# Optimization experiments

Measured on AMD Instinct MI355X. Metric: run time of the kernel, lower is better.

The kernel has to match this reference:

```python
import jax, jax.numpy as jnp
import numpy as np

R_SELF = 0.1  # config.r_self from the 'GENERAL' preset


def setup_inputs() -> dict:
    key = jax.random.key(0)
    k1, k2 = jax.random.split(key)
    N, M, D = 16384, 8192, 128
    x = jax.random.uniform(k1, (N, D), dtype=jnp.float32)
    self_samples = jax.random.uniform(k2, (M, D), dtype=jnp.float32)
    return {"x": x, "self_samples": self_samples}


def _cdist(a, b):
    # Euclidean pairwise distances, same math as torch.cdist(p=2).
    a2 = jnp.sum(a * a, axis=1, keepdims=True)          # [N,1]
    b2 = jnp.sum(b * b, axis=1)[None, :]                # [1,M]
    d2 = a2 + b2 - 2.0 * (a @ b.T)                      # [N,M]
    return jnp.sqrt(jnp.maximum(d2, 0.0))


def reference(x, self_samples):
    # get_anomaly_score: min over self set, shifted by r_self, clamped at 0.
    min_dist_to_self = jnp.min(_cdist(x, self_samples), axis=1)  # [N]
    score = jnp.maximum(min_dist_to_self - R_SELF, 0.0)
    return score
```

## Files before the change

kernel.cpp:

```cpp
#include <hip/hip_runtime.h>


using half_t = _Float16;
typedef _Float16 half8 __attribute__((ext_vector_type(8)));
typedef float floatx16 __attribute__((ext_vector_type(16)));

#define TILE_ELEMS (128 * 128)

__device__ __forceinline__ void async_load16(const void* g, void* l) {
    __builtin_amdgcn_global_load_lds(
        (const __attribute__((address_space(1))) void*)g,
        (__attribute__((address_space(3))) void*)l, 16, 0, 0);
}

__global__ __launch_bounds__(256) void prep_kernel(
    const float* __restrict__ x, const float* __restrict__ self,
    half_t* __restrict__ Aws, half_t* __restrict__ Bws,
    float* __restrict__ b2h, float* __restrict__ a2, int Atiles)
{
    __shared__ float part[256];
    int tile = blockIdx.x;
    int tid  = threadIdx.x;
    bool isB = tile >= Atiles;
    int bt   = tile - Atiles;
    const float* src = isB ? (self + (size_t)bt * TILE_ELEMS)
                           : (x    + (size_t)tile * TILE_ELEMS);
    half_t* dst = isB ? (Bws + (size_t)bt * TILE_ELEMS)
                      : (Aws + (size_t)tile * TILE_ELEMS);
    float sgn = isB ? 1.f : -1.f;

    int rowt = tid & 127;
    int k8b  = tid >> 7;
    float ss = 0.f;
    #pragma unroll
    for (int i = 0; i < 8; ++i) {
        int k8 = i * 2 + k8b;
        const float4* p = (const float4*)(src + rowt * 128 + k8 * 8);
        float4 f0 = p[0];
        float4 f1 = p[1];
        half8 h;
        h[0] = (half_t)(sgn * f0.x); h[1] = (half_t)(sgn * f0.y);
        h[2] = (half_t)(sgn * f0.z); h[3] = (half_t)(sgn * f0.w);
        h[4] = (half_t)(sgn * f1.x); h[5] = (half_t)(sgn * f1.y);
        h[6] = (half_t)(sgn * f1.z); h[7] = (half_t)(sgn * f1.w);
        *(half8*)(dst + (size_t)(i * 256 + tid) * 8) = h;
        ss += f0.x*f0.x + f0.y*f0.y + f0.z*f0.z + f0.w*f0.w;
        ss += f1.x*f1.x + f1.y*f1.y + f1.z*f1.z + f1.w*f1.w;
    }
    part[tid] = ss;
    __syncthreads();
    if (tid < 128) {
        float tot = part[tid] + part[tid + 128];
        if (isB) b2h[bt * 128 + tid] = 0.5f * tot;
        else     a2[tile * 128 + tid] = tot;
    }
}

__global__ __launch_bounds__(256, 2) void min_gemm_kernel(
    const half_t* __restrict__ Aws, const half_t* __restrict__ Bws,
    const float* __restrict__ b2h, float* __restrict__ Pmin,
    int Mslice)
{
    __shared__ half_t Bsh[2][TILE_ELEMS];

    int tid  = threadIdx.x;
    int lane = tid & 63;
    int wid  = tid >> 6;
    int wr   = wid >> 1, wc = wid & 1;
    int ln31 = lane & 31, lh = lane >> 5;

    const half_t* Atile = Aws + (size_t)blockIdx.x * TILE_ELEMS;
    half8 areg[2][8];
    #pragma unroll
    for (int rt = 0; rt < 2; ++rt)
        #pragma unroll
        for (int ki = 0; ki < 8; ++ki) {
            int k8  = ki * 2 + lh;
            int row = wr * 64 + rt * 32 + ln31;
            areg[rt][ki] = *(const half8*)(Atile + (size_t)(k8 * 128 + row) * 8);
        }

    float minacc[2][16];
    #pragma unroll
    for (int rt = 0; rt < 2; ++rt)
        #pragma unroll
        for (int r = 0; r < 16; ++r) minacc[rt][r] = 1e30f;

    int iters = Mslice >> 7;
    int s = blockIdx.y;
    const half_t* Bbase = Bws + (size_t)s * iters * TILE_ELEMS;

    #pragma unroll
    for (int j = 0; j < 8; ++j) {
        int seg = wid * 8 + j;
        async_load16(Bbase + (size_t)(seg * 64 + lane) * 8,
                     &Bsh[0][(size_t)seg * 512]);
    }
    __syncthreads();

    float b2v0 = b2h[s * Mslice + wc * 64 + ln31];
    float b2v1 = b2h[s * Mslice + wc * 64 + 32 + ln31];

    int cur = 0;
    for (int it = 0; it < iters; ++it) {
        if (it + 1 < iters) {
            const half_t* Bt = Bbase + (size_t)(it + 1) * TILE_ELEMS;
            #pragma unroll
            for (int j = 0; j < 8; ++j) {
                int seg = wid * 8 + j;
                async_load16(Bt + (size_t)(seg * 64 + lane) * 8,
                             &Bsh[cur ^ 1][(size_t)seg * 512]);
            }
        }
        int nit = (it + 1 < iters) ? it + 1 : it;
        float nb0 = b2h[s * Mslice + nit * 128 + wc * 64 + ln31];
        float nb1 = b2h[s * Mslice + nit * 128 + wc * 64 + 32 + ln31];

        floatx16 c0, c1;
        #pragma unroll
        for (int r = 0; r < 16; ++r) { c0[r] = b2v0; c1[r] = b2v1; }

        const half_t* Bs = &Bsh[cur][0];

        floatx16 acc00, acc01, acc10, acc11;
        {
            int k8 = lh;
            half8 bf0 = *(const half8*)(Bs + (size_t)(k8 * 128 + wc * 64 + ln31) * 8);
            half8 bf1 = *(const half8*)(Bs + (size_t)(k8 * 128 + wc * 64 + 32 + ln31) * 8);
            acc00 = __builtin_amdgcn_mfma_f32_32x32x16_f16(areg[0][0], bf0, c0, 0, 0, 0);
            acc01 = __builtin_amdgcn_mfma_f32_32x32x16_f16(areg[0][0], bf1, c1, 0, 0, 0);
            acc10 = __builtin_amdgcn_mfma_f32_32x32x16_f16(areg[1][0], bf0, c0, 0, 0, 0);
            acc11 = __builtin_amdgcn_mfma_f32_32x32x16_f16(areg[1][0], bf1, c1, 0, 0, 0);
        }
        #pragma unroll
        for (int ki = 1; ki < 8; ++ki) {
            int k8 = ki * 2 + lh;
            half8 bf0 = *(const half8*)(Bs + (size_t)(k8 * 128 + wc * 64 + ln31) * 8);
            half8 bf1 = *(const half8*)(Bs + (size_t)(k8 * 128 + wc * 64 + 32 + ln31) * 8);
            acc00 = __builtin_amdgcn_mfma_f32_32x32x16_f16(areg[0][ki], bf0, acc00, 0, 0, 0);
            acc01 = __builtin_amdgcn_mfma_f32_32x32x16_f16(areg[0][ki], bf1, acc01, 0, 0, 0);
            acc10 = __builtin_amdgcn_mfma_f32_32x32x16_f16(areg[1][ki], bf0, acc10, 0, 0, 0);
            acc11 = __builtin_amdgcn_mfma_f32_32x32x16_f16(areg[1][ki], bf1, acc11, 0, 0, 0);
        }

        #pragma unroll
        for (int r = 0; r < 16; ++r) {
            minacc[0][r] = fminf(fminf(acc00[r], acc01[r]), minacc[0][r]);
            minacc[1][r] = fminf(fminf(acc10[r], acc11[r]), minacc[1][r]);
        }

        b2v0 = nb0; b2v1 = nb1;

        __syncthreads();
        cur ^= 1;
    }

    #pragma unroll
    for (int rt = 0; rt < 2; ++rt)
        #pragma unroll
        for (int r = 0; r < 16; ++r) {
            float v = minacc[rt][r];
            #pragma unroll
            for (int m = 1; m < 32; m <<= 1)
                v = fminf(v, __shfl_xor(v, m, 64));
            if (ln31 == 0) {
                int row = blockIdx.x * 128 + wr * 64 + rt * 32
                        + (r & 3) + 8 * (r >> 2) + 4 * lh;
                Pmin[(size_t)row * 8 + s * 2 + wc] = v;
            }
        }
}

__global__ __launch_bounds__(256) void final_kernel(
    const float* __restrict__ a2, const float* __restrict__ Pmin,
    float* __restrict__ out)
{
    int row = blockIdx.x * 256 + threadIdx.x;
    const float4* pp = (const float4*)(Pmin + (size_t)row * 8);
    float4 p0 = pp[0];
    float4 p1 = pp[1];
    float p = fminf(fminf(fminf(p0.x, p0.y), fminf(p0.z, p0.w)),
                    fminf(fminf(p1.x, p1.y), fminf(p1.z, p1.w)));
    float d2 = a2[row] + 2.f * p;
    float d  = sqrtf(fmaxf(d2, 0.f));
    out[row] = fmaxf(d - 0.1f, 0.f);
}

extern "C" void kernel_launch(void* const* d_in, const int* in_sizes, int n_in,
                              void* d_out, int out_size, void* d_ws, size_t ws_size,
                              hipStream_t stream)
{
    const float* x    = (const float*)d_in[0];
    const float* self = (const float*)d_in[1];
    float* out        = (float*)d_out;

    int N = in_sizes[0] / 128;
    int M = in_sizes[1] / 128;
    int Atiles = N / 128;
    int Btiles = M / 128;

    char* w      = (char*)d_ws;
    half_t* Aws  = (half_t*)w;
    half_t* Bws  = Aws + (size_t)N * 128;
    float*  b2h  = (float*)(w + (size_t)(N + M) * 128 * 2);
    float*  Pmin = b2h + M;
    float*  a2   = Pmin + (size_t)N * 8;

    prep_kernel<<<Atiles + Btiles, 256, 0, stream>>>(x, self, Aws, Bws, b2h, a2, Atiles);

    int Mslice = M / 4;
    dim3 grid(Atiles, 4);
    min_gemm_kernel<<<grid, 256, 0, stream>>>(Aws, Bws, b2h, Pmin, Mslice);

    final_kernel<<<N / 256, 256, 0, stream>>>(a2, Pmin, out);
}
```

Baseline: 102.3 us.

## Load B fragments directly from global into registers, dropping LDS double buffer

Removes the shared-memory double-buffered B tile staging (async global-to-LDS loads plus barriers) and has each wave read its B fragments straight from global memory into registers each iteration. This eliminates LDS traffic and block-wide synchronisation, and frees 64KB of LDS per block, which could allow more resident blocks. In exchange, B is fetched redundantly by the waves that share columns and is no longer prefetched ahead of use, so global and cache latency is exposed unless occupancy hides it.

Measured after the change: 114.0 us. 11.4% more time.

```diff
diff --git a/kernel.cpp b/kernel.cpp
--- a/kernel.cpp
+++ b/kernel.cpp
@@ -6,12 +6,6 @@
 typedef float floatx16 __attribute__((ext_vector_type(16)));
 
 #define TILE_ELEMS (128 * 128)
-
-__device__ __forceinline__ void async_load16(const void* g, void* l) {
-    __builtin_amdgcn_global_load_lds(
-        (const __attribute__((address_space(1))) void*)g,
-        (__attribute__((address_space(3))) void*)l, 16, 0, 0);
-}
 
 __global__ __launch_bounds__(256) void prep_kernel(
     const float* __restrict__ x, const float* __restrict__ self,
@@ -61,8 +55,6 @@
     const float* __restrict__ b2h, float* __restrict__ Pmin,
     int Mslice)
 {
-    __shared__ half_t Bsh[2][TILE_ELEMS];
-
     int tid  = threadIdx.x;
     int lane = tid & 63;
     int wid  = tid >> 6;
@@ -90,57 +82,36 @@
     int s = blockIdx.y;
     const half_t* Bbase = Bws + (size_t)s * iters * TILE_ELEMS;
 
-    #pragma unroll
-    for (int j = 0; j < 8; ++j) {
-        int seg = wid * 8 + j;
-        async_load16(Bbase + (size_t)(seg * 64 + lane) * 8,
-                     &Bsh[0][(size_t)seg * 512]);
-    }
-    __syncthreads();
+    for (int it = 0; it < iters; ++it) {
+        const half_t* Bt = Bbase + (size_t)it * TILE_ELEMS;
 
-    float b2v0 = b2h[s * Mslice + wc * 64 + ln31];
-    float b2v1 = b2h[s * Mslice + wc * 64 + 32 + ln31];
+        half8 bf0[8], bf1[8];
+        #pragma unroll
+        for (int ki = 0; ki < 8; ++ki) {
+            int k8 = ki * 2 + lh;
+            bf0[ki] = *(const half8*)(Bt + (size_t)(k8 * 128 + wc * 64 + ln31) * 8);
+            bf1[ki] = *(const half8*)(Bt + (size_t)(k8 * 128 + wc * 64 + 32 + ln31) * 8);
+        }
 
-    int cur = 0;
-    for (int it = 0; it < iters; ++it) {
-        if (it + 1 < iters) {
-            const half_t* Bt = Bbase + (size_t)(it + 1) * TILE_ELEMS;
-            #pragma unroll
-            for (int j = 0; j < 8; ++j) {
-                int seg = wid * 8 + j;
-                async_load16(Bt + (size_t)(seg * 64 + lane) * 8,
-                             &Bsh[cur ^ 1][(size_t)seg * 512]);
-            }
-        }
-        int nit = (it + 1 < iters) ? it + 1 : it;
-        float nb0 = b2h[s * Mslice + nit * 128 + wc * 64 + ln31];
-        float nb1 = b2h[s * Mslice + nit * 128 + wc * 64 + 32 + ln31];
+        int colbase = s * Mslice + it * 128 + wc * 64 + ln31;
+        float b2v0 = b2h[colbase];
+        float b2v1 = b2h[colbase + 32];
 
         floatx16 c0, c1;
         #pragma unroll
         for (int r = 0; r < 16; ++r) { c0[r] = b2v0; c1[r] = b2v1; }
 
-        const half_t* Bs = &Bsh[cur][0];
-
         floatx16 acc00, acc01, acc10, acc11;
-        {
-            int k8 = lh;
-            half8 bf0 = *(const half8*)(Bs + (size_t)(k8 * 128 + wc * 64 + ln31) * 8);
-            half8 bf1 = *(const half8*)(Bs + (size_t)(k8 * 128 + wc * 64 + 32 + ln31) * 8);
-            acc00 = __builtin_amdgcn_mfma_f32_32x32x16_f16(areg[0][0], bf0, c0, 0, 0, 0);
-            acc01 = __builtin_amdgcn_mfma_f32_32x32x16_f16(areg[0][0], bf1, c1, 0, 0, 0);
-            acc10 = __builtin_amdgcn_mfma_f32_32x32x16_f16(areg[1][0], bf0, c0, 0, 0, 0);
-            acc11 = __builtin_amdgcn_mfma_f32_32x32x16_f16(areg[1][0], bf1, c1, 0, 0, 0);
-        }
+        acc00 = __builtin_amdgcn_mfma_f32_32x32x16_f16(areg[0][0], bf0[0], c0, 0, 0, 0);
+        acc01 = __builtin_amdgcn_mfma_f32_32x32x16_f16(areg[0][0], bf1[0], c1, 0, 0, 0);
+        acc10 = __builtin_amdgcn_mfma_f32_32x32x16_f16(areg[1][0], bf0[0], c0, 0, 0, 0);
+        acc11 = __builtin_amdgcn_mfma_f32_32x32x16_f16(areg[1][0], bf1[0], c1, 0, 0, 0);
         #pragma unroll
         for (int ki = 1; ki < 8; ++ki) {
-            int k8 = ki * 2 + lh;
-            half8 bf0 = *(const half8*)(Bs + (size_t)(k8 * 128 + wc * 64 + ln31) * 8);
-            half8 bf1 = *(const half8*)(Bs + (size_t)(k8 * 128 + wc * 64 + 32 + ln31) * 8);
-            acc00 = __builtin_amdgcn_mfma_f32_32x32x16_f16(areg[0][ki], bf0, acc00, 0, 0, 0);
-            acc01 = __builtin_amdgcn_mfma_f32_32x32x16_f16(areg[0][ki], bf1, acc01, 0, 0, 0);
-            acc10 = __builtin_amdgcn_mfma_f32_32x32x16_f16(areg[1][ki], bf0, acc10, 0, 0, 0);
-            acc11 = __builtin_amdgcn_mfma_f32_32x32x16_f16(areg[1][ki], bf1, acc11, 0, 0, 0);
+            acc00 = __builtin_amdgcn_mfma_f32_32x32x16_f16(areg[0][ki], bf0[ki], acc00, 0, 0, 0);
+            acc01 = __builtin_amdgcn_mfma_f32_32x32x16_f16(areg[0][ki], bf1[ki], acc01, 0, 0, 0);
+            acc10 = __builtin_amdgcn_mfma_f32_32x32x16_f16(areg[1][ki], bf0[ki], acc10, 0, 0, 0);
+            acc11 = __builtin_amdgcn_mfma_f32_32x32x16_f16(areg[1][ki], bf1[ki], acc11, 0, 0, 0);
         }
 
         #pragma unroll
@@ -148,11 +119,6 @@
             minacc[0][r] = fminf(fminf(acc00[r], acc01[r]), minacc[0][r]);
             minacc[1][r] = fminf(fminf(acc10[r], acc11[r]), minacc[1][r]);
         }
-
-        b2v0 = nb0; b2v1 = nb1;
-
-        __syncthreads();
-        cur ^= 1;
     }
 
     #pragma unroll
```

## Use 512-thread blocks sharing B tiles via a triple-buffered LDS ring

Applied to the files above, without the earlier changes.

Each block now covers 256 A rows with 8 waves, so every staged B tile serves twice as many rows, which halves B traffic per row. B tiles go through a 3-deep LDS ring with explicit vmcnt waits and a single barrier per iteration, keeping two tiles in flight. The b2 slice is also preloaded into LDS once per block. In exchange, LDS use rises to about 104KB per block, which can limit occupancy to one block per CU despite launch_bounds(512,2).

Measured after the change: 100.2 us. 2.1% less time.

```diff
diff --git a/kernel.cpp b/kernel.cpp
--- a/kernel.cpp
+++ b/kernel.cpp
@@ -11,6 +11,15 @@
     __builtin_amdgcn_global_load_lds(
         (const __attribute__((address_space(1))) void*)g,
         (__attribute__((address_space(3))) void*)l, 16, 0, 0);
+}
+
+__device__ __forceinline__ void stage_tile(const half_t* __restrict__ Bt,
+                                           half_t* __restrict__ dst, int tid) {
+    #pragma unroll
+    for (int j = 0; j < 4; ++j) {
+        int chunk = j * 512 + tid;
+        async_load16(Bt + (size_t)chunk * 8, dst + (size_t)chunk * 8);
+    }
 }
 
 __global__ __launch_bounds__(256) void prep_kernel(
@@ -56,12 +65,63 @@
     }
 }
 
-__global__ __launch_bounds__(256, 2) void min_gemm_kernel(
+template<int VN>
+__device__ __forceinline__ void gemm_iter(
+    int t, int iters, int tid, int wc, int ln31, int lh,
+    const half_t* __restrict__ Bbase, half_t (*ring)[TILE_ELEMS],
+    const float* __restrict__ b2sh,
+    const half8 (&areg)[2][8], float (&minacc)[2][16])
+{
+    __builtin_amdgcn_sched_barrier(0);
+    if constexpr (VN == 4) asm volatile("s_waitcnt vmcnt(4)" ::: "memory");
+    else                   asm volatile("s_waitcnt vmcnt(0)" ::: "memory");
+    asm volatile("s_waitcnt lgkmcnt(0)" ::: "memory");
+    __builtin_amdgcn_s_barrier();
+    __builtin_amdgcn_sched_barrier(0);
+
+    if (t + 2 < iters)
+        stage_tile(Bbase + (size_t)(t + 2) * TILE_ELEMS, &ring[(t + 2) % 3][0], tid);
+
+    const half_t* Bs = &ring[t % 3][0];
+    float b2v0 = b2sh[t * 128 + wc * 64 + ln31];
+    float b2v1 = b2sh[t * 128 + wc * 64 + 32 + ln31];
+
+    floatx16 c0, c1;
+    #pragma unroll
+    for (int r = 0; r < 16; ++r) { c0[r] = b2v0; c1[r] = b2v1; }
+
+    floatx16 acc00, acc01, acc10, acc11;
+    {
+        half8 bf0 = *(const half8*)(Bs + (size_t)(lh * 128 + wc * 64 + ln31) * 8);
+        half8 bf1 = *(const half8*)(Bs + (size_t)(lh * 128 + wc * 64 + 32 + ln31) * 8);
+        acc00 = __builtin_amdgcn_mfma_f32_32x32x16_f16(areg[0][0], bf0, c0, 0, 0, 0);
+        acc01 = __builtin_amdgcn_mfma_f32_32x32x16_f16(areg[0][0], bf1, c1, 0, 0, 0);
+        acc10 = __builtin_amdgcn_mfma_f32_32x32x16_f16(areg[1][0], bf0, c0, 0, 0, 0);
+        acc11 = __builtin_amdgcn_mfma_f32_32x32x16_f16(areg[1][0], bf1, c1, 0, 0, 0);
+    }
+    #pragma unroll
+    for (int ki = 1; ki < 8; ++ki) {
+        half8 bf0 = *(const half8*)(Bs + (size_t)((ki * 2 + lh) * 128 + wc * 64 + ln31) * 8);
+        half8 bf1 = *(const half8*)(Bs + (size_t)((ki * 2 + lh) * 128 + wc * 64 + 32 + ln31) * 8);
+        acc00 = __builtin_amdgcn_mfma_f32_32x32x16_f16(areg[0][ki], bf0, acc00, 0, 0, 0);
+        acc01 = __builtin_amdgcn_mfma_f32_32x32x16_f16(areg[0][ki], bf1, acc01, 0, 0, 0);
+        acc10 = __builtin_amdgcn_mfma_f32_32x32x16_f16(areg[1][ki], bf0, acc10, 0, 0, 0);
+        acc11 = __builtin_amdgcn_mfma_f32_32x32x16_f16(areg[1][ki], bf1, acc11, 0, 0, 0);
+    }
+
+    #pragma unroll
+    for (int r = 0; r < 16; ++r) {
+        minacc[0][r] = fminf(fminf(acc00[r], acc01[r]), minacc[0][r]);
+        minacc[1][r] = fminf(fminf(acc10[r], acc11[r]), minacc[1][r]);
+    }
+}
+
+__global__ __launch_bounds__(512, 2) void min_gemm_kernel(
     const half_t* __restrict__ Aws, const half_t* __restrict__ Bws,
-    const float* __restrict__ b2h, float* __restrict__ Pmin,
-    int Mslice)
-{
-    __shared__ half_t Bsh[2][TILE_ELEMS];
+    const float* __restrict__ b2h, float* __restrict__ Pmin, int Mslice)
+{
+    __shared__ half_t ring[3][TILE_ELEMS];
+    __shared__ float  b2sh[2048];
 
     int tid  = threadIdx.x;
     int lane = tid & 63;
@@ -69,16 +129,19 @@
     int wr   = wid >> 1, wc = wid & 1;
     int ln31 = lane & 31, lh = lane >> 5;
 
-    const half_t* Atile = Aws + (size_t)blockIdx.x * TILE_ELEMS;
+    const half_t* Atile = Aws + (size_t)(blockIdx.x * 2 + (wr >> 1)) * TILE_ELEMS;
+    int rbase = (wr & 1) * 64;
     half8 areg[2][8];
     #pragma unroll
     for (int rt = 0; rt < 2; ++rt)
         #pragma unroll
-        for (int ki = 0; ki < 8; ++ki) {
-            int k8  = ki * 2 + lh;
-            int row = wr * 64 + rt * 32 + ln31;
-            areg[rt][ki] = *(const half8*)(Atile + (size_t)(k8 * 128 + row) * 8);
-        }
+        for (int ki = 0; ki < 8; ++ki)
+            areg[rt][ki] = *(const half8*)(
+                Atile + (size_t)((ki * 2 + lh) * 128 + rbase + rt * 32 + ln31) * 8);
+
+    int s = blockIdx.y;
+    for (int j = tid; j < Mslice; j += 512)
+        b2sh[j] = b2h[s * Mslice + j];
 
     float minacc[2][16];
     #pragma unroll
@@ -87,73 +150,16 @@
         for (int r = 0; r < 16; ++r) minacc[rt][r] = 1e30f;
 
     int iters = Mslice >> 7;
-    int s = blockIdx.y;
     const half_t* Bbase = Bws + (size_t)s * iters * TILE_ELEMS;
 
-    #pragma unroll
-    for (int j = 0; j < 8; ++j) {
-        int seg = wid * 8 + j;
-        async_load16(Bbase + (size_t)(seg * 64 + lane) * 8,
-                     &Bsh[0][(size_t)seg * 512]);
-    }
     __syncthreads();
 
-    float b2v0 = b2h[s * Mslice + wc * 64 + ln31];
-    float b2v1 = b2h[s * Mslice + wc * 64 + 32 + ln31];
-
-    int cur = 0;
-    for (int it = 0; it < iters; ++it) {
-        if (it + 1 < iters) {
-            const half_t* Bt = Bbase + (size_t)(it + 1) * TILE_ELEMS;
-            #pragma unroll
-            for (int j = 0; j < 8; ++j) {
-                int seg = wid * 8 + j;
-                async_load16(Bt + (size_t)(seg * 64 + lane) * 8,
-                             &Bsh[cur ^ 1][(size_t)seg * 512]);
-            }
-        }
-        int nit = (it + 1 < iters) ? it + 1 : it;
-        float nb0 = b2h[s * Mslice + nit * 128 + wc * 64 + ln31];
-        float nb1 = b2h[s * Mslice + nit * 128 + wc * 64 + 32 + ln31];
-
-        floatx16 c0, c1;
-        #pragma unroll
-        for (int r = 0; r < 16; ++r) { c0[r] = b2v0; c1[r] = b2v1; }
-
-        const half_t* Bs = &Bsh[cur][0];
-
-        floatx16 acc00, acc01, acc10, acc11;
-        {
-            int k8 = lh;
-            half8 bf0 = *(const half8*)(Bs + (size_t)(k8 * 128 + wc * 64 + ln31) * 8);
-            half8 bf1 = *(const half8*)(Bs + (size_t)(k8 * 128 + wc * 64 + 32 + ln31) * 8);
-            acc00 = __builtin_amdgcn_mfma_f32_32x32x16_f16(areg[0][0], bf0, c0, 0, 0, 0);
-            acc01 = __builtin_amdgcn_mfma_f32_32x32x16_f16(areg[0][0], bf1, c1, 0, 0, 0);
-            acc10 = __builtin_amdgcn_mfma_f32_32x32x16_f16(areg[1][0], bf0, c0, 0, 0, 0);
-            acc11 = __builtin_amdgcn_mfma_f32_32x32x16_f16(areg[1][0], bf1, c1, 0, 0, 0);
-        }
-        #pragma unroll
-        for (int ki = 1; ki < 8; ++ki) {
-            int k8 = ki * 2 + lh;
-            half8 bf0 = *(const half8*)(Bs + (size_t)(k8 * 128 + wc * 64 + ln31) * 8);
-            half8 bf1 = *(const half8*)(Bs + (size_t)(k8 * 128 + wc * 64 + 32 + ln31) * 8);
-            acc00 = __builtin_amdgcn_mfma_f32_32x32x16_f16(areg[0][ki], bf0, acc00, 0, 0, 0);
-            acc01 = __builtin_amdgcn_mfma_f32_32x32x16_f16(areg[0][ki], bf1, acc01, 0, 0, 0);
-            acc10 = __builtin_amdgcn_mfma_f32_32x32x16_f16(areg[1][ki], bf0, acc10, 0, 0, 0);
-            acc11 = __builtin_amdgcn_mfma_f32_32x32x16_f16(areg[1][ki], bf1, acc11, 0, 0, 0);
-        }
-
-        #pragma unroll
-        for (int r = 0; r < 16; ++r) {
-            minacc[0][r] = fminf(fminf(acc00[r], acc01[r]), minacc[0][r]);
-            minacc[1][r] = fminf(fminf(acc10[r], acc11[r]), minacc[1][r]);
-        }
-
-        b2v0 = nb0; b2v1 = nb1;
-
-        __syncthreads();
-        cur ^= 1;
-    }
+    stage_tile(Bbase,              &ring[0][0], tid);
+    stage_tile(Bbase + TILE_ELEMS, &ring[1][0], tid);
+
+    for (int t = 0; t < iters - 1; ++t)
+        gemm_iter<4>(t, iters, tid, wc, ln31, lh, Bbase, ring, b2sh, areg, minacc);
+    gemm_iter<0>(iters - 1, iters, tid, wc, ln31, lh, Bbase, ring, b2sh, areg, minacc);
 
     #pragma unroll
     for (int rt = 0; rt < 2; ++rt)
@@ -164,7 +170,7 @@
             for (int m = 1; m < 32; m <<= 1)
                 v = fminf(v, __shfl_xor(v, m, 64));
             if (ln31 == 0) {
-                int row = blockIdx.x * 128 + wr * 64 + rt * 32
+                int row = blockIdx.x * 256 + wr * 64 + rt * 32
                         + (r & 3) + 8 * (r >> 2) + 4 * lh;
                 Pmin[(size_t)row * 8 + s * 2 + wc] = v;
             }
@@ -209,8 +215,8 @@
     prep_kernel<<<Atiles + Btiles, 256, 0, stream>>>(x, self, Aws, Bws, b2h, a2, Atiles);
 
     int Mslice = M / 4;
-    dim3 grid(Atiles, 4);
-    min_gemm_kernel<<<grid, 256, 0, stream>>>(Aws, Bws, b2h, Pmin, Mslice);
+    dim3 grid(N / 256, 4);
+    min_gemm_kernel<<<grid, 512, 0, stream>>>(Aws, Bws, b2h, Pmin, Mslice);
 
     final_kernel<<<N / 256, 256, 0, stream>>>(a2, Pmin, out);
 }
```
